# Performance work log

Hardware: AMD Instinct MI355X
Metric: run time of the kernel (lower is better)

The kernel has to match this reference:

```python
import jax, jax.numpy as jnp
import numpy as np

N_NODES = 20000
K = 8                      # forward offsets per node; total degree = 2K = 16
IN_FEAT = 128
HID = 256
OUT_FEAT = 1
EPS = 1e-5


def _build_graph():
    # Regular undirected graph: node i -> (i+o) % N for o in 1..K, plus reverse edges.
    base = np.repeat(np.arange(N_NODES), K)
    off = np.tile(np.arange(1, K + 1), N_NODES)
    d = (base + off) % N_NODES
    src = np.concatenate([base, d]).astype(np.int32)   # [E], E = 2*N*K
    dst = np.concatenate([d, base]).astype(np.int32)
    deg = 2 * K
    # Every node has exactly `deg` out-edges and `deg` in-edges -> reshape works.
    out_ids = np.argsort(src, kind='stable').reshape(N_NODES, deg)  # edges leaving v
    in_ids = np.argsort(dst, kind='stable').reshape(N_NODES, deg)   # edges entering v
    # Directed line graph: edge (a,v) -> edge (v,c): pair every in-edge with every out-edge of v.
    line_src = np.repeat(in_ids, deg, axis=1).ravel().astype(np.int32)
    line_dst = np.tile(out_ids, (1, deg)).ravel().astype(np.int32)
    return np.stack([src, dst]), np.stack([line_src, line_dst])


def setup_inputs() -> dict:
    key = jax.random.key(0)
    ks = jax.random.split(key, 4)
    ei, lei = _build_graph()
    x = jax.random.normal(ks[0], (N_NODES, IN_FEAT), jnp.float32)
    W1 = jax.random.normal(ks[1], (IN_FEAT, HID), jnp.float32) / np.sqrt(IN_FEAT).astype(np.float32)
    b1 = jnp.zeros((HID,), jnp.float32)
    gamma1 = jnp.ones((HID,), jnp.float32)
    beta1 = jnp.zeros((HID,), jnp.float32)
    W2 = jax.random.normal(ks[2], (HID, HID), jnp.float32) / np.sqrt(HID).astype(np.float32)
    b2 = jnp.zeros((HID,), jnp.float32)
    Wl = jax.random.normal(ks[3], (2 * HID, OUT_FEAT), jnp.float32) / np.sqrt(2 * HID).astype(np.float32)
    bl = jnp.zeros((OUT_FEAT,), jnp.float32)
    return {"x": x, "W1": W1, "b1": b1, "gamma1": gamma1, "beta1": beta1,
            "W2": W2, "b2": b2, "Wl": Wl, "bl": bl,
            "edge_index": jnp.asarray(ei), "line_edge_index": jnp.asarray(lei)}


def _gcn(x, edge_index, W, b, n):
    # GCNConv: add self loops, symmetric deg^{-1/2} normalization, sum aggregation.
    h = x @ W                                                  # [n, out]
    loops = jnp.arange(n, dtype=edge_index.dtype)
    src = jnp.concatenate([edge_index[0], loops])
    dst = jnp.concatenate([edge_index[1], loops])
    deg = jax.ops.segment_sum(jnp.ones(src.shape, h.dtype), dst, num_segments=n)
    dinv = jnp.where(deg > 0, jax.lax.rsqrt(jnp.maximum(deg, 1.0)), 0.0)
    norm = dinv[src] * dinv[dst]                               # [E+n]
    return jax.ops.segment_sum(h[src] * norm[:, None], dst, num_segments=n) + b


def _batch_norm(x, gamma, beta):
    mu = x.mean(axis=0)
    var = x.var(axis=0)
    return (x - mu) * jax.lax.rsqrt(var + EPS) * gamma + beta


def reference(x, W1, b1, gamma1, beta1, W2, b2, Wl, bl, edge_index, line_edge_index):
    n = x.shape[0]
    h = jax.nn.relu(_batch_norm(_gcn(x, edge_index, W1, b1, n), gamma1, beta1))
    h = jax.nn.relu(_gcn(h, edge_index, W2, b2, n))
    # to_line_graph, node_feat_mixing='cat': one line-node per edge, feat = [x_src | x_dst]
    line_x = jnp.concatenate([h[edge_index[0]], h[edge_index[1]]], axis=1)  # [E, 2*HID]
    out = _gcn(line_x, line_edge_index, Wl, bl, line_x.shape[0])
    return jax.nn.sigmoid(out)
```

## Files before the change

### kernel.cpp

```cpp
#include <hip/hip_runtime.h>
#include <hip/hip_bf16.h>
#include <math.h>

#define NN    20000
#define NK    160000
#define NEDGE 320000
#define HID   256
#define INFEAT 128
#define EPSF  1e-5f
#define NT1   313
#define MOUT  104
#define NT2B  193

typedef __bf16  bf16x8 __attribute__((ext_vector_type(8)));
typedef float   f32x4  __attribute__((ext_vector_type(4)));
typedef ushort  u16x8  __attribute__((ext_vector_type(8)));

__device__ __forceinline__ float sigmoidf_(float x) { return 1.0f / (1.0f + expf(-x)); }

__device__ __forceinline__ ushort f2bf(float f) {
    __hip_bfloat16 h = __float2bfloat16(f);
    return __builtin_bit_cast(ushort, h);
}
__device__ __forceinline__ float bf2f(ushort u) {
    return __builtin_bit_cast(float, ((unsigned int)u) << 16);
}
__device__ __forceinline__ int wrapN(int v) {
    return (v < 0) ? v + NN : ((v >= NN) ? v - NN : v);
}

#define LDSP(p) ((__attribute__((address_space(3))) unsigned int*)(p))
#define GBLP(p) ((const __attribute__((address_space(1))) unsigned int*)(p))
#define GLD16(g, l) __builtin_amdgcn_global_load_lds(GBLP(g), LDSP(l), 16, 0, 0)

__global__ __launch_bounds__(512, 2) void k_prep(const float* __restrict__ W1,
    const float* __restrict__ W2, ushort* __restrict__ W1t,
    ushort* __restrict__ W2t, float* __restrict__ asum)
{
    const int b = blockIdx.x, t = threadIdx.x;
    if (b < 16) {
        const int e = (b * 512 + t) * 4;
        ushort4 o;
        #pragma unroll
        for (int j = 0; j < 4; ++j) {
            const int ee = e + j;
            const int n = ee >> 7, k = ee & 127;
            ((ushort*)&o)[j] = f2bf(W1[k * 256 + n]);
        }
        *reinterpret_cast<ushort4*>(W1t + e) = o;
    } else if (b < 48) {
        const int e = ((b - 16) * 512 + t) * 4;
        ushort4 o;
        #pragma unroll
        for (int j = 0; j < 4; ++j) {
            const int ee = e + j;
            const int n = ee >> 8, k = ee & 255;
            ((ushort*)&o)[j] = f2bf(W2[k * 256 + n]);
        }
        *reinterpret_cast<ushort4*>(W2t + e) = o;
    } else {
        asum[t]       = 0.f;
        asum[512 + t] = 0.f;
    }
}

__global__ __launch_bounds__(512, 2) void k_fused1(const float* __restrict__ x,
    const ushort* __restrict__ W1t, const float* __restrict__ b1,
    ushort* __restrict__ A, float* __restrict__ asum)
{
    __shared__ alignas(16) char smem[21760 + 8192 + 32768];
    char* xr = smem;
    char* As = smem + 21760;
    char* Bs = smem + 21760 + 8192;

    const int t = threadIdx.x;
    const int wave = t >> 6, lane = t & 63;
    const int wr = (wave >> 2) * 32;
    const int wc = (wave & 3) * 32;
    const int bm = blockIdx.x * 64;
    const float inv17 = 1.0f / 17.0f;
    f32x4 acc[2][2][2] = {};

    #pragma unroll
    for (int kt = 0; kt < 2; ++kt) {
        const int k0 = kt * 64;
        #pragma unroll
        for (int it = 0; it < 4; ++it) {
            const int cb = (it * 8 + wave) * 64 + lane;
            const int row = cb >> 3;
            const int lk = (cb & 7) ^ (row & 7);
            GLD16(W1t + (size_t)row * INFEAT + k0 + lk * 8, Bs + (it * 8 + wave) * 1024);
        }
        #pragma unroll
        for (int r3 = 0; r3 < 3; ++r3) {
            const int c = r3 * 512 + t;
            if (c < 1280) {
                const int row = c >> 4, cc = c & 15;
                const int rg = wrapN(bm - 8 + row);
                const float4 v = *reinterpret_cast<const float4*>(
                    x + (size_t)rg * INFEAT + k0 + cc * 4);
                *reinterpret_cast<float4*>(xr + row * 272 + cc * 16) = v;
            }
        }
        __syncthreads();
        {
            const int row = t >> 3, c8 = t & 7;
            float S[8] = {};
            #pragma unroll
            for (int i = 0; i < 17; ++i) {
                const float4 a = *reinterpret_cast<const float4*>(xr + (row + i) * 272 + c8 * 32);
                const float4 bq = *reinterpret_cast<const float4*>(xr + (row + i) * 272 + c8 * 32 + 16);
                S[0] += a.x;  S[1] += a.y;  S[2] += a.z;  S[3] += a.w;
                S[4] += bq.x; S[5] += bq.y; S[6] += bq.z; S[7] += bq.w;
            }
            u16x8 o;
            #pragma unroll
            for (int j = 0; j < 8; ++j) o[j] = f2bf(S[j] * inv17);
            *reinterpret_cast<u16x8*>(As + row * 128 + ((c8 ^ (row & 7)) * 16)) = o;
        }
        __syncthreads();
        #pragma unroll
        for (int kk = 0; kk < 2; ++kk) {
            const int klog = kk * 64 + ((lane >> 4) << 4);
            bf16x8 af[2];
            #pragma unroll
            for (int mi = 0; mi < 2; ++mi) {
                const int row = wr + mi * 16 + (lane & 15);
                af[mi] = *reinterpret_cast<const bf16x8*>(As + row * 128 + (klog ^ ((row & 7) << 4)));
            }
            #pragma unroll
            for (int ny = 0; ny < 2; ++ny)
                #pragma unroll
                for (int ni = 0; ni < 2; ++ni) {
                    const int row = ny * 128 + wc + ni * 16 + (lane & 15);
                    const bf16x8 bv = *reinterpret_cast<const bf16x8*>(Bs + row * 128 + (klog ^ ((row & 7) << 4)));
                    #pragma unroll
                    for (int mi = 0; mi < 2; ++mi)
                        acc[ny][mi][ni] = __builtin_amdgcn_mfma_f32_16x16x32_bf16(af[mi], bv, acc[ny][mi][ni], 0, 0, 0);
                }
        }
        __syncthreads();
    }

    float* sS  = (float*)smem;
    float* s2S = (float*)(smem + 2048);
    #pragma unroll
    for (int ny = 0; ny < 2; ++ny)
        #pragma unroll
        for (int ni = 0; ni < 2; ++ni) {
            const int colL = ny * 128 + wc + ni * 16 + (lane & 15);
            const float bv = b1[colL];
            float sv = 0.f, s2v = 0.f;
            #pragma unroll
            for (int mi = 0; mi < 2; ++mi)
                #pragma unroll
                for (int r = 0; r < 4; ++r) {
                    const int row = bm + wr + mi * 16 + ((lane >> 4) << 2) + r;
                    if (row < NN) {
                        const float val = acc[ny][mi][ni][r] + bv;
                        A[(size_t)row * 256 + colL] = f2bf(val);
                        sv += val; s2v += val * val;
                    }
                }
            sv  += __shfl_xor(sv, 16);  sv  += __shfl_xor(sv, 32);
            s2v += __shfl_xor(s2v, 16); s2v += __shfl_xor(s2v, 32);
            if (lane < 16) {
                sS [wave * 64 + ny * 32 + ni * 16 + lane] = sv;
                s2S[wave * 64 + ny * 32 + ni * 16 + lane] = s2v;
            }
        }
    __syncthreads();
    if (t < 256) {
        const int col = t;
        const int idx = (col >> 7) * 32 + ((col >> 4) & 1) * 16 + (col & 15);
        const int wcx = (col & 127) >> 5;
        atomicAdd(&asum[col],       sS [wcx * 64 + idx] + sS [(wcx + 4) * 64 + idx]);
        atomicAdd(&asum[512 + col], s2S[wcx * 64 + idx] + s2S[(wcx + 4) * 64 + idx]);
    }
}

__global__ __launch_bounds__(512, 2) void k_fused2(const ushort* __restrict__ A,
    const ushort* __restrict__ W2t, const float* __restrict__ gamma,
    const float* __restrict__ beta, const float* __restrict__ b2,
    const float* __restrict__ Wl, const float* __restrict__ bl,
    const float* __restrict__ asum, float* __restrict__ out)
{
    __shared__ alignas(16) char smem[23040 + 16384 + 16384 + 2048];
    char* xr   = smem;
    char* As   = smem + 23040;
    char* Bs   = smem + 23040 + 16384;
    float* ssS = (float*)(smem + 23040 + 16384 + 16384);

    const int b = blockIdx.x, t = threadIdx.x;
    const int wave = t >> 6, lane = t & 63;
    const int wr  = (wave >> 1) * 32;
    const int wcx = (wave & 1);
    const int v0 = b * MOUT;
    const float inv17 = 1.0f / 17.0f;

    if (t < 256) {
        const float invn = 1.0f / (float)NN;
        const float mu  = asum[t] * invn;
        const float var = asum[512 + t] * invn - mu * mu;
        const float sc  = gamma[t] * rsqrtf(var + EPSF);
        ssS[t]       = sc;
        ssS[256 + t] = beta[t] - mu * sc;
    }
    __syncthreads();

    f32x4 acc[2][2][4] = {};

    #pragma unroll
    for (int kt = 0; kt < 4; ++kt) {
        const int k0 = kt * 64;
        #pragma unroll
        for (int it = 0; it < 2; ++it) {
            const int cb = (it * 8 + wave) * 64 + lane;
            const int row = cb >> 3;
            const int lk = (cb & 7) ^ (row & 7);
            GLD16(W2t + (size_t)row * 256 + k0 + lk * 8, Bs + (it * 8 + wave) * 1024);
        }
        #pragma unroll
        for (int r3 = 0; r3 < 3; ++r3) {
            const int c = r3 * 512 + t;
            if (c < 1152) {
                const int row = c >> 3, c8 = c & 7;
                const int rg = wrapN(v0 - 16 + row);
                const int fb = k0 + c8 * 8;
                const u16x8 a = *reinterpret_cast<const u16x8*>(A + (size_t)rg * 256 + fb);
                const float4 sc0 = *reinterpret_cast<const float4*>(ssS + fb);
                const float4 sc1 = *reinterpret_cast<const float4*>(ssS + fb + 4);
                const float4 sh0 = *reinterpret_cast<const float4*>(ssS + 256 + fb);
                const float4 sh1 = *reinterpret_cast<const float4*>(ssS + 256 + fb + 4);
                u16x8 p;
                p[0] = f2bf(fmaxf(bf2f(a[0]) * sc0.x + sh0.x, 0.f));
                p[1] = f2bf(fmaxf(bf2f(a[1]) * sc0.y + sh0.y, 0.f));
                p[2] = f2bf(fmaxf(bf2f(a[2]) * sc0.z + sh0.z, 0.f));
                p[3] = f2bf(fmaxf(bf2f(a[3]) * sc0.w + sh0.w, 0.f));
                p[4] = f2bf(fmaxf(bf2f(a[4]) * sc1.x + sh1.x, 0.f));
                p[5] = f2bf(fmaxf(bf2f(a[5]) * sc1.y + sh1.y, 0.f));
                p[6] = f2bf(fmaxf(bf2f(a[6]) * sc1.z + sh1.z, 0.f));
                p[7] = f2bf(fmaxf(bf2f(a[7]) * sc1.w + sh1.w, 0.f));
                *reinterpret_cast<u16x8*>(xr + row * 160 + c8 * 16) = p;
            }
        }
        __syncthreads();

        u16x8 bq0, bq1;
        {
            const int cb0 = t, cb1 = t + 512;
            bq0 = *reinterpret_cast<const u16x8*>(
                W2t + (size_t)(128 + (cb0 >> 3)) * 256 + k0 + (cb0 & 7) * 8);
            bq1 = *reinterpret_cast<const u16x8*>(
                W2t + (size_t)(128 + (cb1 >> 3)) * 256 + k0 + (cb1 & 7) * 8);
        }

        {
            const int q = t >> 3, c8 = t & 7;
            const int r0 = 2 * q;
            float S[8] = {};
            #pragma unroll
            for (int i = 0; i < 17; ++i) {
                const u16x8 h = *reinterpret_cast<const u16x8*>(xr + (r0 + i) * 160 + c8 * 16);
                #pragma unroll
                for (int j = 0; j < 8; ++j) S[j] += bf2f(h[j]);
            }
            u16x8 o;
            #pragma unroll
            for (int j = 0; j < 8; ++j) o[j] = f2bf(S[j] * inv17);
            *reinterpret_cast<u16x8*>(As + r0 * 128 + ((c8 ^ (r0 & 7)) * 16)) = o;
            const u16x8 ha = *reinterpret_cast<const u16x8*>(xr + (r0 + 17) * 160 + c8 * 16);
            const u16x8 hs = *reinterpret_cast<const u16x8*>(xr + r0 * 160 + c8 * 16);
            #pragma unroll
            for (int j = 0; j < 8; ++j) S[j] += bf2f(ha[j]) - bf2f(hs[j]);
            const int r1 = r0 + 1;
            #pragma unroll
            for (int j = 0; j < 8; ++j) o[j] = f2bf(S[j] * inv17);
            *reinterpret_cast<u16x8*>(As + r1 * 128 + ((c8 ^ (r1 & 7)) * 16)) = o;
        }
        __syncthreads();

        #pragma unroll
        for (int kk = 0; kk < 2; ++kk) {
            const int klog = kk * 64 + ((lane >> 4) << 4);
            bf16x8 af[2];
            #pragma unroll
            for (int mi = 0; mi < 2; ++mi) {
                const int row = wr + mi * 16 + (lane & 15);
                af[mi] = *reinterpret_cast<const bf16x8*>(As + row * 128 + (klog ^ ((row & 7) << 4)));
            }
            #pragma unroll
            for (int ni = 0; ni < 4; ++ni) {
                const int rl = wcx * 64 + ni * 16 + (lane & 15);
                const bf16x8 bv = *reinterpret_cast<const bf16x8*>(Bs + rl * 128 + (klog ^ ((rl & 7) << 4)));
                #pragma unroll
                for (int mi = 0; mi < 2; ++mi)
                    acc[0][mi][ni] = __builtin_amdgcn_mfma_f32_16x16x32_bf16(af[mi], bv, acc[0][mi][ni], 0, 0, 0);
            }
        }
        __syncthreads();

        {
            const int cb0 = t, cb1 = t + 512;
            const int r0w = cb0 >> 3, r1w = cb1 >> 3;
            *reinterpret_cast<u16x8*>(Bs + r0w * 128 + (((cb0 & 7) ^ (r0w & 7)) * 16)) = bq0;
            *reinterpret_cast<u16x8*>(Bs + r1w * 128 + (((cb1 & 7) ^ (r1w & 7)) * 16)) = bq1;
        }
        __syncthreads();

        #pragma unroll
        for (int kk = 0; kk < 2; ++kk) {
            const int klog = kk * 64 + ((lane >> 4) << 4);
            bf16x8 af[2];
            #pragma unroll
            for (int mi = 0; mi < 2; ++mi) {
                const int row = wr + mi * 16 + (lane & 15);
                af[mi] = *reinterpret_cast<const bf16x8*>(As + row * 128 + (klog ^ ((row & 7) << 4)));
            }
            #pragma unroll
            for (int ni = 0; ni < 4; ++ni) {
                const int rl = wcx * 64 + ni * 16 + (lane & 15);
                const bf16x8 bv = *reinterpret_cast<const bf16x8*>(Bs + rl * 128 + (klog ^ ((rl & 7) << 4)));
                #pragma unroll
                for (int mi = 0; mi < 2; ++mi)
                    acc[1][mi][ni] = __builtin_amdgcn_mfma_f32_16x16x32_bf16(af[mi], bv, acc[1][mi][ni], 0, 0, 0);
            }
        }
        __syncthreads();
    }

    float b2v[2][4], wav[2][4], wbv[2][4];
    #pragma unroll
    for (int h = 0; h < 2; ++h)
        #pragma unroll
        for (int ni = 0; ni < 4; ++ni) {
            const int col = h * 128 + wcx * 64 + ni * 16 + (lane & 15);
            b2v[h][ni] = b2[col];
            wav[h][ni] = Wl[col];
            wbv[h][ni] = Wl[256 + col];
        }
    float* uW = (float*)smem;
    float* wW = (float*)(smem + 1024);
    float* uL = (float*)(smem + 23040);
    float* wL = (float*)(smem + 23040 + 512);
    float* PS = (float*)(smem + 23040 + 1024);
    #pragma unroll
    for (int mi = 0; mi < 2; ++mi)
        #pragma unroll
        for (int r = 0; r < 4; ++r) {
            float pu = 0.f, pw = 0.f;
            #pragma unroll
            for (int h = 0; h < 2; ++h)
                #pragma unroll
                for (int ni = 0; ni < 4; ++ni) {
                    const float hv = fmaxf(acc[h][mi][ni][r] + b2v[h][ni], 0.f);
                    pu += hv * wav[h][ni];
                    pw += hv * wbv[h][ni];
                }
            pu += __shfl_xor(pu, 1); pu += __shfl_xor(pu, 2);
            pu += __shfl_xor(pu, 4); pu += __shfl_xor(pu, 8);
            pw += __shfl_xor(pw, 1); pw += __shfl_xor(pw, 2);
            pw += __shfl_xor(pw, 4); pw += __shfl_xor(pw, 8);
            if ((lane & 15) == 0) {
                const int rl = wr + mi * 16 + ((lane >> 4) << 2) + r;
                uW[wcx * 128 + rl] = pu;
                wW[wcx * 128 + rl] = pw;
            }
        }
    __syncthreads();
    if (t < 128) {
        uL[t] = uW[t] + uW[128 + t];
        wL[t] = wW[t] + wW[128 + t];
    }
    __syncthreads();

    if (t < 112) {
        const int l = t + 8;
        float s = uL[l] + 16.0f * wL[l];
        #pragma unroll
        for (int o = 1; o <= 8; ++o)
            s += uL[l + o] + uL[l - o];
        PS[t] = s;
    }
    __syncthreads();

    const float blv = bl[0];
    #pragma unroll
    for (int rr = 0; rr < 4; ++rr) {
        const int q = t + rr * 512;
        if (q >= 1664) continue;
        const int half = (q >= 832) ? 1 : 0;
        const int e = q - half * 832;
        const int i = e >> 3, off = e & 7;
        const int v = v0 + i;
        if (v >= NN) continue;
        if (!half) {
            out[v * 8 + off] = sigmoidf_((PS[i] + wL[i + 9 + off]) * inv17 + blv);
        } else {
            out[NK + v * 8 + off] = sigmoidf_((PS[i + 1 + off] + wL[i + 8]) * inv17 + blv);
        }
    }
}

extern "C" void kernel_launch(void* const* d_in, const int* in_sizes, int n_in,
                              void* d_out, int out_size, void* d_ws, size_t ws_size,
                              hipStream_t stream)
{
    const float* x      = (const float*)d_in[0];
    const float* W1     = (const float*)d_in[1];
    const float* b1     = (const float*)d_in[2];
    const float* gamma1 = (const float*)d_in[3];
    const float* beta1  = (const float*)d_in[4];
    const float* W2     = (const float*)d_in[5];
    const float* b2     = (const float*)d_in[6];
    const float* Wl     = (const float*)d_in[7];
    const float* bl     = (const float*)d_in[8];
    float* out = (float*)d_out;

    float*    asum = (float*)d_ws;
    ushort*   A    = (ushort*)(asum + 1024);
    ushort*   W1t  = A + (size_t)NN * 256;
    ushort*   W2t  = W1t + 256 * 128;

    k_prep  <<<49,   512, 0, stream>>>(W1, W2, W1t, W2t, asum);
    k_fused1<<<NT1,  512, 0, stream>>>(x, W1t, b1, A, asum);
    k_fused2<<<NT2B, 512, 0, stream>>>(A, W2t, gamma1, beta1, b2, Wl, bl, asum, out);
}
```

Before: 48.72 us.

## Use sliding-window aggregation with swizzled staging and full-width W2 tile in LDS

```diff
diff --git a/kernel.cpp b/kernel.cpp
--- a/kernel.cpp
+++ b/kernel.cpp
@@ -96,27 +96,49 @@
             const int c = r3 * 512 + t;
             if (c < 1280) {
                 const int row = c >> 4, cc = c & 15;
+                const int g = cc >> 1, hf = cc & 1;
+                const int pg = g ^ ((row >> 2) & 7);
                 const int rg = wrapN(bm - 8 + row);
                 const float4 v = *reinterpret_cast<const float4*>(
                     x + (size_t)rg * INFEAT + k0 + cc * 4);
-                *reinterpret_cast<float4*>(xr + row * 272 + cc * 16) = v;
-            }
-        }
-        __syncthreads();
-        {
-            const int row = t >> 3, c8 = t & 7;
+                *reinterpret_cast<float4*>(xr + row * 272 + pg * 32 + hf * 16) = v;
+            }
+        }
+        __syncthreads();
+        if (t < 128) {
+            const int q = t >> 3, c8 = t & 7;
+            const int r0 = 4 * q;
             float S[8] = {};
             #pragma unroll
             for (int i = 0; i < 17; ++i) {
-                const float4 a = *reinterpret_cast<const float4*>(xr + (row + i) * 272 + c8 * 32);
-                const float4 bq = *reinterpret_cast<const float4*>(xr + (row + i) * 272 + c8 * 32 + 16);
+                const int r = r0 + i;
+                const char* base = xr + r * 272 + ((c8 ^ ((r >> 2) & 7)) * 32);
+                const float4 a  = *reinterpret_cast<const float4*>(base);
+                const float4 bq = *reinterpret_cast<const float4*>(base + 16);
                 S[0] += a.x;  S[1] += a.y;  S[2] += a.z;  S[3] += a.w;
                 S[4] += bq.x; S[5] += bq.y; S[6] += bq.z; S[7] += bq.w;
             }
-            u16x8 o;
-            #pragma unroll
-            for (int j = 0; j < 8; ++j) o[j] = f2bf(S[j] * inv17);
-            *reinterpret_cast<u16x8*>(As + row * 128 + ((c8 ^ (row & 7)) * 16)) = o;
+            #pragma unroll
+            for (int jr = 0; jr < 4; ++jr) {
+                const int l = r0 + jr;
+                u16x8 o;
+                #pragma unroll
+                for (int j = 0; j < 8; ++j) o[j] = f2bf(S[j] * inv17);
+                *reinterpret_cast<u16x8*>(As + l * 128 + ((c8 ^ (l & 7)) * 16)) = o;
+                if (jr < 3) {
+                    const int ra = l + 17, rs = l;
+                    const char* ba = xr + ra * 272 + ((c8 ^ ((ra >> 2) & 7)) * 32);
+                    const char* bs = xr + rs * 272 + ((c8 ^ ((rs >> 2) & 7)) * 32);
+                    const float4 a0 = *reinterpret_cast<const float4*>(ba);
+                    const float4 a1 = *reinterpret_cast<const float4*>(ba + 16);
+                    const float4 s0 = *reinterpret_cast<const float4*>(bs);
+                    const float4 s1 = *reinterpret_cast<const float4*>(bs + 16);
+                    S[0] += a0.x - s0.x; S[1] += a0.y - s0.y;
+                    S[2] += a0.z - s0.z; S[3] += a0.w - s0.w;
+                    S[4] += a1.x - s1.x; S[5] += a1.y - s1.y;
+                    S[6] += a1.z - s1.z; S[7] += a1.w - s1.w;
+                }
+            }
         }
         __syncthreads();
         #pragma unroll
@@ -185,11 +207,11 @@
     const float* __restrict__ Wl, const float* __restrict__ bl,
     const float* __restrict__ asum, float* __restrict__ out)
 {
-    __shared__ alignas(16) char smem[23040 + 16384 + 16384 + 2048];
+    __shared__ alignas(16) char smem[23040 + 16384 + 32768 + 2048];
     char* xr   = smem;
     char* As   = smem + 23040;
     char* Bs   = smem + 23040 + 16384;
-    float* ssS = (float*)(smem + 23040 + 16384 + 16384);
+    float* ssS = (float*)(smem + 23040 + 16384 + 32768);
 
     const int b = blockIdx.x, t = threadIdx.x;
     const int wave = t >> 6, lane = t & 63;
@@ -214,7 +236,7 @@
     for (int kt = 0; kt < 4; ++kt) {
         const int k0 = kt * 64;
         #pragma unroll
-        for (int it = 0; it < 2; ++it) {
+        for (int it = 0; it < 4; ++it) {
             const int cb = (it * 8 + wave) * 64 + lane;
             const int row = cb >> 3;
             const int lk = (cb & 7) ^ (row & 7);
@@ -225,6 +247,7 @@
             const int c = r3 * 512 + t;
             if (c < 1152) {
                 const int row = c >> 3, c8 = c & 7;
+                const int pc8 = c8 ^ ((row >> 3) & 7);
                 const int rg = wrapN(v0 - 16 + row);
                 const int fb = k0 + c8 * 8;
                 const u16x8 a = *reinterpret_cast<const u16x8*>(A + (size_t)rg * 256 + fb);
@@ -241,45 +264,41 @@
                 p[5] = f2bf(fmaxf(bf2f(a[5]) * sc1.y + sh1.y, 0.f));
                 p[6] = f2bf(fmaxf(bf2f(a[6]) * sc1.z + sh1.z, 0.f));
                 p[7] = f2bf(fmaxf(bf2f(a[7]) * sc1.w + sh1.w, 0.f));
-                *reinterpret_cast<u16x8*>(xr + row * 160 + c8 * 16) = p;
-            }
-        }
-        __syncthreads();
-
-        u16x8 bq0, bq1;
-        {
-            const int cb0 = t, cb1 = t + 512;
-            bq0 = *reinterpret_cast<const u16x8*>(
-                W2t + (size_t)(128 + (cb0 >> 3)) * 256 + k0 + (cb0 & 7) * 8);
-            bq1 = *reinterpret_cast<const u16x8*>(
-                W2t + (size_t)(128 + (cb1 >> 3)) * 256 + k0 + (cb1 & 7) * 8);
-        }
-
-        {
+                *reinterpret_cast<u16x8*>(xr + row * 160 + pc8 * 16) = p;
+            }
+        }
+        __syncthreads();
+        if (t < 128) {
             const int q = t >> 3, c8 = t & 7;
-            const int r0 = 2 * q;
+            const int r0 = 8 * q;
             float S[8] = {};
             #pragma unroll
             for (int i = 0; i < 17; ++i) {
-                const u16x8 h = *reinterpret_cast<const u16x8*>(xr + (r0 + i) * 160 + c8 * 16);
+                const int r = r0 + i;
+                const u16x8 h = *reinterpret_cast<const u16x8*>(
+                    xr + r * 160 + ((c8 ^ ((r >> 3) & 7)) * 16));
                 #pragma unroll
                 for (int j = 0; j < 8; ++j) S[j] += bf2f(h[j]);
             }
-            u16x8 o;
-            #pragma unroll
-            for (int j = 0; j < 8; ++j) o[j] = f2bf(S[j] * inv17);
-            *reinterpret_cast<u16x8*>(As + r0 * 128 + ((c8 ^ (r0 & 7)) * 16)) = o;
-            const u16x8 ha = *reinterpret_cast<const u16x8*>(xr + (r0 + 17) * 160 + c8 * 16);
-            const u16x8 hs = *reinterpret_cast<const u16x8*>(xr + r0 * 160 + c8 * 16);
-            #pragma unroll
-            for (int j = 0; j < 8; ++j) S[j] += bf2f(ha[j]) - bf2f(hs[j]);
-            const int r1 = r0 + 1;
-            #pragma unroll
-            for (int j = 0; j < 8; ++j) o[j] = f2bf(S[j] * inv17);
-            *reinterpret_cast<u16x8*>(As + r1 * 128 + ((c8 ^ (r1 & 7)) * 16)) = o;
-        }
-        __syncthreads();
-
+            #pragma unroll
+            for (int jr = 0; jr < 8; ++jr) {
+                const int l = r0 + jr;
+                u16x8 o;
+                #pragma unroll
+                for (int j = 0; j < 8; ++j) o[j] = f2bf(S[j] * inv17);
+                *reinterpret_cast<u16x8*>(As + l * 128 + ((c8 ^ (l & 7)) * 16)) = o;
+                if (jr < 7) {
+                    const int ra = l + 17, rs = l;
+                    const u16x8 ha = *reinterpret_cast<const u16x8*>(
+                        xr + ra * 160 + ((c8 ^ ((ra >> 3) & 7)) * 16));
+                    const u16x8 hs = *reinterpret_cast<const u16x8*>(
+                        xr + rs * 160 + ((c8 ^ ((rs >> 3) & 7)) * 16));
+                    #pragma unroll
+                    for (int j = 0; j < 8; ++j) S[j] += bf2f(ha[j]) - bf2f(hs[j]);
+                }
+            }
+        }
+        __syncthreads();
         #pragma unroll
         for (int kk = 0; kk < 2; ++kk) {
             const int klog = kk * 64 + ((lane >> 4) << 4);
@@ -290,41 +309,15 @@
                 af[mi] = *reinterpret_cast<const bf16x8*>(As + row * 128 + (klog ^ ((row & 7) << 4)));
             }
             #pragma unroll
-            for (int ni = 0; ni < 4; ++ni) {
-                const int rl = wcx * 64 + ni * 16 + (lane & 15);
-                const bf16x8 bv = *reinterpret_cast<const bf16x8*>(Bs + rl * 128 + (klog ^ ((rl & 7) << 4)));
-                #pragma unroll
-                for (int mi = 0; mi < 2; ++mi)
-                    acc[0][mi][ni] = __builtin_amdgcn_mfma_f32_16x16x32_bf16(af[mi], bv, acc[0][mi][ni], 0, 0, 0);
-            }
-        }
-        __syncthreads();
-
-        {
-            const int cb0 = t, cb1 = t + 512;
-            const int r0w = cb0 >> 3, r1w = cb1 >> 3;
-            *reinterpret_cast<u16x8*>(Bs + r0w * 128 + (((cb0 & 7) ^ (r0w & 7)) * 16)) = bq0;
-            *reinterpret_cast<u16x8*>(Bs + r1w * 128 + (((cb1 & 7) ^ (r1w & 7)) * 16)) = bq1;
-        }
-        __syncthreads();
-
-        #pragma unroll
-        for (int kk = 0; kk < 2; ++kk) {
-            const int klog = kk * 64 + ((lane >> 4) << 4);
-            bf16x8 af[2];
-            #pragma unroll
-            for (int mi = 0; mi < 2; ++mi) {
-                const int row = wr + mi * 16 + (lane & 15);
-                af[mi] = *reinterpret_cast<const bf16x8*>(As + row * 128 + (klog ^ ((row & 7) << 4)));
-            }
-            #pragma unroll
-            for (int ni = 0; ni < 4; ++ni) {
-                const int rl = wcx * 64 + ni * 16 + (lane & 15);
-                const bf16x8 bv = *reinterpret_cast<const bf16x8*>(Bs + rl * 128 + (klog ^ ((rl & 7) << 4)));
-                #pragma unroll
-                for (int mi = 0; mi < 2; ++mi)
-                    acc[1][mi][ni] = __builtin_amdgcn_mfma_f32_16x16x32_bf16(af[mi], bv, acc[1][mi][ni], 0, 0, 0);
-            }
+            for (int h = 0; h < 2; ++h)
+                #pragma unroll
+                for (int ni = 0; ni < 4; ++ni) {
+                    const int rl = h * 128 + wcx * 64 + ni * 16 + (lane & 15);
+                    const bf16x8 bv = *reinterpret_cast<const bf16x8*>(Bs + rl * 128 + (klog ^ ((rl & 7) << 4)));
+                    #pragma unroll
+                    for (int mi = 0; mi < 2; ++mi)
+                        acc[h][mi][ni] = __builtin_amdgcn_mfma_f32_16x16x32_bf16(af[mi], bv, acc[h][mi][ni], 0, 0, 0);
+                }
         }
         __syncthreads();
     }
```

Result: slower. 56.04 us (+15.0%).
